# Kernel tuning notes

Measured on AMD Instinct MI355X. Metric: run time of the kernel, lower is better.

Reference implementation:

```python
import jax, jax.numpy as jnp
import numpy as np

EPS = 8.0 / 255.0  # hparams['epsilon']


def setup_inputs() -> dict:
    key = jax.random.key(0)
    k1, k2, k3, k4 = jax.random.split(key, 4)
    B, N, C, H, Wd, K = 128, 96, 3, 32, 32, 10
    D = C * H * Wd
    imgs = jax.random.uniform(k1, (B, C, H, Wd), dtype=jnp.float32)
    # sample_deltas: uniform in [-eps, eps]
    deltas = 2.0 * EPS * jax.random.uniform(k2, (N, B, C, H, Wd), dtype=jnp.float32) - EPS
    W = jax.random.normal(k3, (D, K), dtype=jnp.float32) * (1.0 / np.sqrt(D))
    b = jnp.zeros((K,), dtype=jnp.float32)
    labels = jax.random.randint(k4, (B,), 0, K, dtype=jnp.int32)
    ind = 91  # math.ceil(N * proportion) - 1 with N=96, proportion=0.95
    return {"imgs": imgs, "deltas": deltas, "W": W, "b": b, "labels": labels, "ind": ind}


def reference(imgs, deltas, W, b, labels, ind):
    N, B = deltas.shape[:2]
    # pert_imgs = clamp(imgs + delta, 0, 1), flattened for the linear classifier
    x = jnp.clip(imgs[None] + deltas, 0.0, 1.0).reshape(N, B, -1)  # [N,B,D]
    logits = jnp.einsum('nbd,dk->nbk', x, W) + b                    # [N,B,K]
    logp = jax.nn.log_softmax(logits, axis=-1)
    # pert_loss1 = CE(logits, labels), per-sample
    loss1 = -jnp.take_along_axis(logp, labels[None, :, None], axis=-1)[..., 0]  # [N,B]
    # top-2 labels; new_labels = second-best class
    _, top2 = jax.lax.top_k(logits, 2)
    top1, second = top2[..., 0], top2[..., 1]
    loss2 = -jnp.take_along_axis(logp, second[..., None], axis=-1)[..., 0]      # [N,B]
    # mask: if argmax != label, pert_loss2[i] = -10000
    loss2 = jnp.where(top1 == labels[None, :], loss2, jnp.float32(-10000.0))
    # layout [B,N] as in torch.cat(..., dim=1)
    l1 = loss1.T
    l2 = loss2.T
    order = jnp.argsort(l1 - l2, axis=1)                 # sort(loss1 - loss2) indices
    sel_idx = order[:, ind]                              # per-sample selected column
    # torch.tensor(list) detaches -> no gradient through selected losses
    selected = jax.lax.stop_gradient(jnp.take_along_axis(l2, sel_idx[:, None], axis=1))  # [B,1]
    robust_loss = jnp.mean(jnp.mean(l1 - selected, axis=1))
    return robust_loss
```

## Files before the change

kernel.cpp:

```cpp
#include <hip/hip_runtime.h>
#include <hip/hip_bf16.h>
#include <math.h>

#define BB 128
#define NN 96
#define DD 3072
#define KK 10
#define SPL 8
#define KST 12

typedef short s16x8 __attribute__((ext_vector_type(8)));
typedef float f32x4 __attribute__((ext_vector_type(4)));

__global__ __launch_bounds__(256) void k0_pack(
    const float* __restrict__ W, unsigned short* __restrict__ pwg,
    unsigned int* __restrict__ counter)
{
    if (blockIdx.x == 0 && threadIdx.x == 0) *counter = 0u;
    const int r = blockIdx.x * 256 + threadIdx.x;
    const int col  = r & 15;
    const int quad = (r >> 4) & 3;
    const int kb   = r >> 6;
    union { unsigned short us[8]; uint4 v; } rec;
#pragma unroll
    for (int j = 0; j < 8; ++j) {
        const int k = kb * 32 + quad * 8 + j;
        const float v = (col < KK) ? W[k * KK + col] : 0.0f;
        const __hip_bfloat16 h = __float2bfloat16(v);
        __builtin_memcpy(&rec.us[j], &h, 2);
    }
    ((uint4*)pwg)[r] = rec.v;
}

__global__ __launch_bounds__(512) void k1_mfma(
    const float* __restrict__ imgs,
    const float* __restrict__ deltas,
    const unsigned short* __restrict__ pwg,
    const float* __restrict__ bias,
    const int*   __restrict__ labels,
    float* __restrict__ l1_ws,
    float* __restrict__ l2_ws)
{
    const int lane = threadIdx.x & 63;
    const int wv   = threadIdx.x >> 6;
    const int tile = blockIdx.x;
    const int r0   = tile * 16;
    const int n    = r0 >> 7;
    const int b0   = r0 & 127;
    const int m    = lane & 15;
    const int quad = lane >> 4;

    const float* ap = deltas + (size_t)(r0 + m) * DD + wv * (KST * 32) + quad * 8;
    const float* ip = imgs   + (size_t)(b0 + m) * DD + wv * (KST * 32) + quad * 8;
    const unsigned short* wp = pwg + ((size_t)(wv * KST) * 64 + lane) * 8;

    f32x4 acc = {0.f, 0.f, 0.f, 0.f};
#pragma unroll 2
    for (int s = 0; s < KST; ++s) {
        const float4 d0 = *(const float4*)(ap);
        const float4 d1 = *(const float4*)(ap + 4);
        const float4 i0 = *(const float4*)(ip);
        const float4 i1 = *(const float4*)(ip + 4);
        const s16x8 bfrag = *(const s16x8*)(wp);
        float x[8];
        x[0] = d0.x + i0.x; x[1] = d0.y + i0.y; x[2] = d0.z + i0.z; x[3] = d0.w + i0.w;
        x[4] = d1.x + i1.x; x[5] = d1.y + i1.y; x[6] = d1.z + i1.z; x[7] = d1.w + i1.w;
        s16x8 afrag;
#pragma unroll
        for (int j = 0; j < 8; ++j) {
            const float xc = fminf(fmaxf(x[j], 0.f), 1.f);
            const __hip_bfloat16 h = __float2bfloat16(xc);
            unsigned short us; __builtin_memcpy(&us, &h, 2);
            afrag[j] = (short)us;
        }
        acc = __builtin_amdgcn_mfma_f32_16x16x32_bf16(afrag, bfrag, acc, 0, 0, 0);
        ap += 32; ip += 32; wp += 512;
    }

    __shared__ float sred[SPL][16][16];
#pragma unroll
    for (int reg = 0; reg < 4; ++reg)
        sred[wv][quad * 4 + reg][m] = acc[reg];
    __syncthreads();

    if (wv == 0 && lane < 16) {
        const int rr = lane;
        float lg[KK];
#pragma unroll
        for (int k = 0; k < KK; ++k) {
            float s = 0.f;
#pragma unroll
            for (int sp = 0; sp < SPL; ++sp) s += sred[sp][rr][k];
            lg[k] = s + bias[k];
        }
        int top1 = 0; float m1 = lg[0];
#pragma unroll
        for (int k = 1; k < KK; ++k) if (lg[k] > m1) { m1 = lg[k]; top1 = k; }
        int sec = (top1 == 0) ? 1 : 0; float m2 = lg[sec];
#pragma unroll
        for (int k = 0; k < KK; ++k)
            if (k != top1 && lg[k] > m2) { m2 = lg[k]; sec = k; }
        float se = 0.f;
#pragma unroll
        for (int k = 0; k < KK; ++k) se += expf(lg[k] - m1);
        const float lse = m1 + logf(se);
        const int b = b0 + rr;
        const int lab = labels[b];
        const float loss1 = lse - lg[lab];
        const float loss2 = (top1 == lab) ? (lse - lg[sec]) : -10000.0f;
        l1_ws[b * NN + n] = loss1;
        l2_ws[b * NN + n] = loss2;
    }
}

__global__ __launch_bounds__(128) void k2_select(
    const float* __restrict__ l1_ws, const float* __restrict__ l2_ws,
    const int* __restrict__ ind_p, float* __restrict__ perb,
    unsigned int* __restrict__ counter, float* __restrict__ out)
{
    const int b = blockIdx.x;
    const int t = threadIdx.x;
    __shared__ float sd[NN];
    __shared__ float sl2[NN];
    __shared__ float ssel;
    __shared__ float swsum[2];
    __shared__ unsigned int slast;

    float myl1 = 0.f, myd = 0.f;
    if (t < NN) {
        const float a = l1_ws[b * NN + t];
        const float c = l2_ws[b * NN + t];
        myl1 = a; myd = a - c;
        sd[t] = myd; sl2[t] = c;
    }
    __syncthreads();

    if (t < NN) {
        int rank = 0;
        for (int j = 0; j < NN; ++j) {
            const float dj = sd[j];
            rank += (dj < myd) || (dj == myd && j < t);
        }
        if (rank == ind_p[0]) ssel = sl2[t];
    }

    float s = myl1;
#pragma unroll
    for (int off = 32; off >= 1; off >>= 1) s += __shfl_down(s, off, 64);
    if ((t & 63) == 0) swsum[t >> 6] = s;
    __syncthreads();
    if (t == 0) {
        const float total = swsum[0] + swsum[1];
        perb[b] = total / 96.0f - ssel;
        __threadfence();
        const unsigned int prev = atomicAdd(counter, 1u);
        slast = (prev == BB - 1) ? 1u : 0u;
    }
    __syncthreads();

    if (slast) {
        __threadfence();
        float v = perb[t];
#pragma unroll
        for (int off = 32; off >= 1; off >>= 1) v += __shfl_down(v, off, 64);
        if ((t & 63) == 0) swsum[t >> 6] = v;
        __syncthreads();
        if (t == 0) out[0] = (swsum[0] + swsum[1]) / 128.0f;
    }
}

extern "C" void kernel_launch(void* const* d_in, const int* in_sizes, int n_in,
                              void* d_out, int out_size, void* d_ws, size_t ws_size,
                              hipStream_t stream) {
    const float* imgs   = (const float*)d_in[0];
    const float* deltas = (const float*)d_in[1];
    const float* W      = (const float*)d_in[2];
    const float* bias   = (const float*)d_in[3];
    const int*   labels = (const int*)d_in[4];
    const int*   ind    = (const int*)d_in[5];
    float* out = (float*)d_out;

    float* l1_ws = (float*)d_ws;
    float* l2_ws = l1_ws + NN * BB;
    float* perb  = l2_ws + NN * BB;
    unsigned int* counter = (unsigned int*)(perb + BB);
    unsigned short* pwg = (unsigned short*)(counter + 4);

    k0_pack<<<dim3(24), dim3(256), 0, stream>>>(W, pwg, counter);
    k1_mfma<<<dim3(768), dim3(512), 0, stream>>>(
        imgs, deltas, pwg, bias, labels, l1_ws, l2_ws);
    k2_select<<<dim3(BB), dim3(128), 0, stream>>>(
        l1_ws, l2_ws, ind, perb, counter, out);
}
```

Baseline: 240.8 us.

## Stage deltas through double-buffered LDS with coalesced chunked loads in MFMA kernel

The MFMA kernel now loads delta rows in contiguous 256-float chunks per tile row, with fully coalesced 16-byte loads into a double-buffered shared-memory tile. Waves then read their MFMA fragments from LDS, and the K dimension is interleaved across waves per chunk instead of split into contiguous per-wave ranges. The goal is better DRAM coalescing on the dominant deltas stream, plus prefetching the next chunk while computing the current one. The cost is a block-wide barrier every iteration and extra LDS traffic.

```diff
diff --git a/kernel.cpp b/kernel.cpp
--- a/kernel.cpp
+++ b/kernel.cpp
@@ -7,7 +7,8 @@
 #define DD 3072
 #define KK 10
 #define SPL 8
-#define KST 12
+#define W_CH 256
+#define NCH 12
 
 typedef short s16x8 __attribute__((ext_vector_type(8)));
 typedef float f32x4 __attribute__((ext_vector_type(4)));
@@ -50,34 +51,64 @@
     const int m    = lane & 15;
     const int quad = lane >> 4;
 
-    const float* ap = deltas + (size_t)(r0 + m) * DD + wv * (KST * 32) + quad * 8;
-    const float* ip = imgs   + (size_t)(b0 + m) * DD + wv * (KST * 32) + quad * 8;
-    const unsigned short* wp = pwg + ((size_t)(wv * KST) * 64 + lane) * 8;
+    __shared__ float ldsD[2][16][W_CH];
+    __shared__ float sred[SPL][16][16];
+
+    const int rec0  = wv * 128 + lane;
+    const int rec1  = rec0 + 64;
+    const int srow0 = rec0 >> 6, scol0 = rec0 & 63;
+    const int srow1 = rec1 >> 6, scol1 = rec1 & 63;
+    const float* gs0 = deltas + (size_t)(r0 + srow0) * DD + scol0 * 4;
+    const float* gs1 = deltas + (size_t)(r0 + srow1) * DD + scol1 * 4;
+
+    const float* ipb = imgs + (size_t)(b0 + m) * DD + wv * 32 + quad * 8;
+    const unsigned short* wpb = pwg + ((size_t)wv * 64 + lane) * 8;
+    const int uf = wv * 32 + quad * 8;
+
+    {
+        const f32x4 s0 = *(const f32x4*)(gs0);
+        const f32x4 s1 = *(const f32x4*)(gs1);
+        *(f32x4*)&ldsD[0][srow0][scol0 * 4] = s0;
+        *(f32x4*)&ldsD[0][srow1][scol1 * 4] = s1;
+    }
+    __syncthreads();
 
     f32x4 acc = {0.f, 0.f, 0.f, 0.f};
 #pragma unroll 2
-    for (int s = 0; s < KST; ++s) {
-        const float4 d0 = *(const float4*)(ap);
-        const float4 d1 = *(const float4*)(ap + 4);
-        const float4 i0 = *(const float4*)(ip);
-        const float4 i1 = *(const float4*)(ip + 4);
-        const s16x8 bfrag = *(const s16x8*)(wp);
-        float x[8];
-        x[0] = d0.x + i0.x; x[1] = d0.y + i0.y; x[2] = d0.z + i0.z; x[3] = d0.w + i0.w;
-        x[4] = d1.x + i1.x; x[5] = d1.y + i1.y; x[6] = d1.z + i1.z; x[7] = d1.w + i1.w;
+    for (int c = 0; c < NCH; ++c) {
+        const int cb = c & 1;
+        f32x4 t0, t1;
+        const bool more = (c + 1 < NCH);
+        if (more) {
+            t0 = *(const f32x4*)(gs0 + (c + 1) * W_CH);
+            t1 = *(const f32x4*)(gs1 + (c + 1) * W_CH);
+        }
+        const f32x4 dv0 = *(const f32x4*)&ldsD[cb][m][uf];
+        const f32x4 dv1 = *(const f32x4*)&ldsD[cb][m][uf + 4];
+        const f32x4 iv0 = *(const f32x4*)(ipb + c * W_CH);
+        const f32x4 iv1 = *(const f32x4*)(ipb + c * W_CH + 4);
+        const s16x8 bfrag = *(const s16x8*)(wpb + (size_t)c * 4096);
         s16x8 afrag;
 #pragma unroll
-        for (int j = 0; j < 8; ++j) {
-            const float xc = fminf(fmaxf(x[j], 0.f), 1.f);
-            const __hip_bfloat16 h = __float2bfloat16(xc);
-            unsigned short us; __builtin_memcpy(&us, &h, 2);
-            afrag[j] = (short)us;
+        for (int j = 0; j < 4; ++j) {
+            const float xc0 = fminf(fmaxf(dv0[j] + iv0[j], 0.f), 1.f);
+            const float xc1 = fminf(fmaxf(dv1[j] + iv1[j], 0.f), 1.f);
+            const __hip_bfloat16 h0 = __float2bfloat16(xc0);
+            const __hip_bfloat16 h1 = __float2bfloat16(xc1);
+            unsigned short us0, us1;
+            __builtin_memcpy(&us0, &h0, 2);
+            __builtin_memcpy(&us1, &h1, 2);
+            afrag[j]     = (short)us0;
+            afrag[j + 4] = (short)us1;
         }
         acc = __builtin_amdgcn_mfma_f32_16x16x32_bf16(afrag, bfrag, acc, 0, 0, 0);
-        ap += 32; ip += 32; wp += 512;
-    }
-
-    __shared__ float sred[SPL][16][16];
+        if (more) {
+            *(f32x4*)&ldsD[cb ^ 1][srow0][scol0 * 4] = t0;
+            *(f32x4*)&ldsD[cb ^ 1][srow1][scol1 * 4] = t1;
+        }
+        __syncthreads();
+    }
+
 #pragma unroll
     for (int reg = 0; reg < 4; ++reg)
         sred[wv][quad * 4 + reg][m] = acc[reg];
```

After: 242.0 us. Within noise of the previous version (+0.5%).

## Split input conversion into streaming pre-pass writing bf16 MFMA fragments

Applied to the files above, without the earlier changes.

Adds a streaming kernel that reads deltas and imgs contiguously, clamps and converts them to bf16, and stores them pre-laid-out in MFMA A-fragment order; the W packing is folded into it. The MFMA kernel then loads ready fragments instead of doing strided fp32 loads plus conversion. The aim is more coalesced, higher-bandwidth reads of the large deltas tensor, at the cost of writing and re-reading an intermediate buffer about half the size of the input.

```diff
diff --git a/kernel.cpp b/kernel.cpp
--- a/kernel.cpp
+++ b/kernel.cpp
@@ -8,33 +8,71 @@
 #define KK 10
 #define SPL 8
 #define KST 12
+#define H_TOT (NN * BB * 384)
+#define H_STRIDE (2048 * 256)
 
 typedef short s16x8 __attribute__((ext_vector_type(8)));
 typedef float f32x4 __attribute__((ext_vector_type(4)));
 
-__global__ __launch_bounds__(256) void k0_pack(
-    const float* __restrict__ W, unsigned short* __restrict__ pwg,
+__global__ __launch_bounds__(256) void k1a_stream(
+    const float* __restrict__ imgs,
+    const float* __restrict__ deltas,
+    const float* __restrict__ W,
+    unsigned short* __restrict__ pwg,
+    unsigned short* __restrict__ xp,
     unsigned int* __restrict__ counter)
 {
     if (blockIdx.x == 0 && threadIdx.x == 0) *counter = 0u;
-    const int r = blockIdx.x * 256 + threadIdx.x;
-    const int col  = r & 15;
-    const int quad = (r >> 4) & 3;
-    const int kb   = r >> 6;
-    union { unsigned short us[8]; uint4 v; } rec;
-#pragma unroll
-    for (int j = 0; j < 8; ++j) {
-        const int k = kb * 32 + quad * 8 + j;
-        const float v = (col < KK) ? W[k * KK + col] : 0.0f;
-        const __hip_bfloat16 h = __float2bfloat16(v);
-        __builtin_memcpy(&rec.us[j], &h, 2);
-    }
-    ((uint4*)pwg)[r] = rec.v;
-}
-
-__global__ __launch_bounds__(512) void k1_mfma(
-    const float* __restrict__ imgs,
-    const float* __restrict__ deltas,
+    if (blockIdx.x < 24) {
+        const int r = blockIdx.x * 256 + threadIdx.x;
+        const int col  = r & 15;
+        const int quad = (r >> 4) & 3;
+        const int kb   = r >> 6;
+        union { unsigned short us[8]; uint4 v; } rec;
+#pragma unroll
+        for (int j = 0; j < 8; ++j) {
+            const int k = kb * 32 + quad * 8 + j;
+            const float v = (col < KK) ? W[k * KK + col] : 0.0f;
+            const __hip_bfloat16 h = __float2bfloat16(v);
+            __builtin_memcpy(&rec.us[j], &h, 2);
+        }
+        ((uint4*)pwg)[r] = rec.v;
+    }
+
+    int h = blockIdx.x * 256 + threadIdx.x;
+#pragma unroll 1
+    for (int it = 0; it < 9; ++it, h += H_STRIDE) {
+        const int row = h / 384;
+        const int d8  = h - row * 384;
+        const float* dp = deltas + (size_t)h * 8;
+        const float* ip = imgs + (size_t)(row & 127) * DD + d8 * 8;
+        const f32x4 da = *(const f32x4*)(dp);
+        const f32x4 db = *(const f32x4*)(dp + 4);
+        const f32x4 ia = *(const f32x4*)(ip);
+        const f32x4 ib = *(const f32x4*)(ip + 4);
+        s16x8 afrag;
+#pragma unroll
+        for (int j = 0; j < 4; ++j) {
+            const float x0 = fminf(fmaxf(da[j] + ia[j], 0.f), 1.f);
+            const float x1 = fminf(fmaxf(db[j] + ib[j], 0.f), 1.f);
+            const __hip_bfloat16 h0 = __float2bfloat16(x0);
+            const __hip_bfloat16 h1 = __float2bfloat16(x1);
+            unsigned short us0, us1;
+            __builtin_memcpy(&us0, &h0, 2);
+            __builtin_memcpy(&us1, &h1, 2);
+            afrag[j]     = (short)us0;
+            afrag[j + 4] = (short)us1;
+        }
+        const int tile = row >> 4;
+        const int m    = row & 15;
+        const int sg   = d8 >> 2;
+        const int q    = d8 & 3;
+        *(s16x8*)(xp + (((size_t)tile * 96 + sg) * 64 + (q * 16 + m)) * 8) = afrag;
+    }
+}
+
+__global__ __launch_bounds__(512) void k1b_mfma(
+    const unsigned short* __restrict__ xp,
     const unsigned short* __restrict__ pwg,
     const float* __restrict__ bias,
     const int*   __restrict__ labels,
@@ -50,31 +88,16 @@
     const int m    = lane & 15;
     const int quad = lane >> 4;
 
-    const float* ap = deltas + (size_t)(r0 + m) * DD + wv * (KST * 32) + quad * 8;
-    const float* ip = imgs   + (size_t)(b0 + m) * DD + wv * (KST * 32) + quad * 8;
+    const unsigned short* ap = xp + (((size_t)tile * 96 + wv * KST) * 64 + lane) * 8;
     const unsigned short* wp = pwg + ((size_t)(wv * KST) * 64 + lane) * 8;
 
     f32x4 acc = {0.f, 0.f, 0.f, 0.f};
 #pragma unroll 2
     for (int s = 0; s < KST; ++s) {
-        const float4 d0 = *(const float4*)(ap);
-        const float4 d1 = *(const float4*)(ap + 4);
-        const float4 i0 = *(const float4*)(ip);
-        const float4 i1 = *(const float4*)(ip + 4);
+        const s16x8 afrag = *(const s16x8*)(ap);
         const s16x8 bfrag = *(const s16x8*)(wp);
-        float x[8];
-        x[0] = d0.x + i0.x; x[1] = d0.y + i0.y; x[2] = d0.z + i0.z; x[3] = d0.w + i0.w;
-        x[4] = d1.x + i1.x; x[5] = d1.y + i1.y; x[6] = d1.z + i1.z; x[7] = d1.w + i1.w;
-        s16x8 afrag;
-#pragma unroll
-        for (int j = 0; j < 8; ++j) {
-            const float xc = fminf(fmaxf(x[j], 0.f), 1.f);
-            const __hip_bfloat16 h = __float2bfloat16(xc);
-            unsigned short us; __builtin_memcpy(&us, &h, 2);
-            afrag[j] = (short)us;
-        }
         acc = __builtin_amdgcn_mfma_f32_16x16x32_bf16(afrag, bfrag, acc, 0, 0, 0);
-        ap += 32; ip += 32; wp += 512;
+        ap += 512; wp += 512;
     }
 
     __shared__ float sred[SPL][16][16];
@@ -185,10 +208,12 @@
     float* perb  = l2_ws + NN * BB;
     unsigned int* counter = (unsigned int*)(perb + BB);
     unsigned short* pwg = (unsigned short*)(counter + 4);
-
-    k0_pack<<<dim3(24), dim3(256), 0, stream>>>(W, pwg, counter);
-    k1_mfma<<<dim3(768), dim3(512), 0, stream>>>(
-        imgs, deltas, pwg, bias, labels, l1_ws, l2_ws);
+    unsigned short* xp  = pwg + (size_t)6144 * 8;
+
+    k1a_stream<<<dim3(2048), dim3(256), 0, stream>>>(
+        imgs, deltas, W, pwg, xp, counter);
+    k1b_mfma<<<dim3(768), dim3(512), 0, stream>>>(
+        xp, pwg, bias, labels, l1_ws, l2_ws);
     k2_select<<<dim3(BB), dim3(128), 0, stream>>>(
         l1_ws, l2_ws, ind, perb, counter, out);
 }
```

Result: slower. 299.0 us (+24.1%).
